# Kernel optimization log

Hardware: AMD Instinct MI355X
Metric: run time of the kernel (lower is better)

Reference implementation:

```python
import jax, jax.numpy as jnp
import numpy as np

# dims
B, N, DEG = 128, 512, 8          # graphs per batch, nodes per graph, avg degree
NL, F1, F2, F3 = 32, 128, 96, 64  # label dim, GCN filter sizes
K, BINS, BN = 16, 16, 32          # tensor_neurons, bins, bottle_neck_neurons
NT = B * N                        # total nodes per side
E = NT * DEG                      # total edges per side


def setup_inputs() -> dict:
    key = jax.random.key(0)
    ks = jax.random.split(key, 24)
    x1 = jax.random.normal(ks[0], (NT, NL), jnp.float32)
    x2 = jax.random.normal(ks[1], (NT, NL), jnp.float32)
    # edges constrained to stay within each graph's node block
    src1 = jax.random.randint(ks[2], (E,), 0, NT)
    dst1 = (src1 // N) * N + jax.random.randint(ks[3], (E,), 0, N)
    src2 = jax.random.randint(ks[4], (E,), 0, NT)
    dst2 = (src2 // N) * N + jax.random.randint(ks[5], (E,), 0, N)
    edge_index_1 = jnp.stack([src1, dst1]).astype(jnp.int32)
    edge_index_2 = jnp.stack([src2, dst2]).astype(jnp.int32)
    batch = jnp.repeat(jnp.arange(B, dtype=jnp.int32), N)
    s = 0.1
    params = dict(
        Wc1=jax.random.normal(ks[6], (NL, F1), jnp.float32) * s,
        bc1=jnp.zeros((F1,), jnp.float32),
        Wc2=jax.random.normal(ks[7], (F1, F2), jnp.float32) * s,
        bc2=jnp.zeros((F2,), jnp.float32),
        Wc3=jax.random.normal(ks[8], (F2, F3), jnp.float32) * s,
        bc3=jnp.zeros((F3,), jnp.float32),
        Watt=jax.random.normal(ks[9], (F3, F3), jnp.float32) * s,
        Wt=jax.random.normal(ks[10], (F3, F3, K), jnp.float32) * s,
        Wtb=jax.random.normal(ks[11], (K, 2 * F3), jnp.float32) * s,
        tb=jnp.zeros((K,), jnp.float32),
        W1=jax.random.normal(ks[12], (K + BINS, BN), jnp.float32) * s,
        b1=jnp.zeros((BN,), jnp.float32),
        Ws=jax.random.normal(ks[13], (BN, 1), jnp.float32) * s,
        bs=jnp.zeros((1,), jnp.float32),
    )
    return dict(x1=x1, x2=x2, edge_index_1=edge_index_1, edge_index_2=edge_index_2,
                batch_1=batch, batch_2=batch, **params)


def gcn_layer(x, src, dst, W, b):
    # PyG GCNConv: out = D^{-1/2}(A+I)D^{-1/2} (x W) + b
    n = x.shape[0]
    deg = jax.ops.segment_sum(jnp.ones(src.shape[0], x.dtype), dst, num_segments=n) + 1.0
    dinv = jax.lax.rsqrt(deg)
    h = x @ W
    norm = dinv[src] * dinv[dst]
    agg = jax.ops.segment_sum(h[src] * norm[:, None], dst, num_segments=n)
    agg = agg + h * (dinv * dinv)[:, None]  # self-loop term
    return agg + b


def conv_pass(x, src, dst, Wc1, bc1, Wc2, bc2, Wc3, bc3):
    h = jax.nn.relu(gcn_layer(x, src, dst, Wc1, bc1))  # dropout is identity in eval
    h = jax.nn.relu(gcn_layer(h, src, dst, Wc2, bc2))
    return gcn_layer(h, src, dst, Wc3, bc3)


def attention_pool(x, batch, Watt):
    # SimGNN attention: sigmoid(x . tanh(mean_g(x) W)) weighted sum per graph
    cnt = jax.ops.segment_sum(jnp.ones(x.shape[0], x.dtype), batch, num_segments=B)
    mean = jax.ops.segment_sum(x, batch, num_segments=B) / cnt[:, None]
    ctx = jnp.tanh(mean @ Watt)                       # [B, F3]
    coef = jax.nn.sigmoid(jnp.sum(x * ctx[batch], -1))  # [NT]
    return jax.ops.segment_sum(x * coef[:, None], batch, num_segments=B)


def histogram(f1, f2):
    # all graphs have exactly N nodes -> dense batch is a reshape, num_nodes=N
    f1d = f1.reshape(B, N, F3)
    f2d = f2.reshape(B, N, F3)
    s = jax.lax.stop_gradient(jnp.einsum('bnf,bmf->bnm', f1d, f2d))  # detach
    v = jax.nn.sigmoid(s).reshape(B, N * N)
    vmin = v.min(1, keepdims=True)
    vmax = v.max(1, keepdims=True)
    width = (vmax - vmin) / BINS  # torch.histc with min=max=0 uses data range
    safe = jnp.where(width > 0, width, 1.0)
    idx = jnp.clip(jnp.floor((v - vmin) / safe), 0, BINS - 1).astype(jnp.int32)
    flat = (idx + jnp.arange(B, dtype=jnp.int32)[:, None] * BINS).reshape(-1)
    hist = jax.ops.segment_sum(jnp.ones(B * N * N, v.dtype), flat,
                               num_segments=B * BINS).reshape(B, BINS)
    return hist / hist.sum(1, keepdims=True)


def reference(x1, x2, edge_index_1, edge_index_2, batch_1, batch_2,
              Wc1, bc1, Wc2, bc2, Wc3, bc3, Watt, Wt, Wtb, tb, W1, b1, Ws, bs):
    f1 = conv_pass(x1, edge_index_1[0], edge_index_1[1], Wc1, bc1, Wc2, bc2, Wc3, bc3)
    f2 = conv_pass(x2, edge_index_2[0], edge_index_2[1], Wc1, bc1, Wc2, bc2, Wc3, bc3)
    hist = histogram(f1, f2)
    p1 = attention_pool(f1, batch_1, Watt)
    p2 = attention_pool(f2, batch_2, Watt)
    # tensor network: e1^T W[:,:,k] e2 + Wtb [e1;e2] + b
    scoring = jnp.einsum('bi,ijk,bj->bk', p1, Wt, p2)
    block = jnp.concatenate([p1, p2], axis=1) @ Wtb.T
    t = jax.nn.relu(scoring + block + tb)             # [B, K]
    feat = jnp.concatenate([t, hist], axis=1)         # [B, K+BINS]
    h = jax.nn.relu(feat @ W1 + b1)
    return jax.nn.sigmoid(h @ Ws + bs).reshape(-1)    # [B]
```

## Files before the change

### kernel.cpp

```cpp
#include <hip/hip_runtime.h>
#include <math.h>

#define NTOT  65536
#define NEDGE 524288
#define BGR   128
#define NPG   512
#define NL    32
#define F1    128
#define F2    96
#define F3    64
#define KT    16
#define BINS  16
#define BN    32
#define GCAP  6144

typedef unsigned short bf;
typedef __attribute__((ext_vector_type(8))) short sv8;
typedef __attribute__((ext_vector_type(16))) float fv16;

__device__ __forceinline__ float b2f(bf v) { return __uint_as_float(((unsigned)v) << 16); }
__device__ __forceinline__ bf f2b(float f) {
    unsigned u = __float_as_uint(f);
    return (bf)((u + 0x7FFF + ((u >> 16) & 1)) >> 16);
}
__device__ __forceinline__ float sigm(float x) { return 1.f / (1.f + expf(-x)); }

__global__ __launch_bounds__(256) void init_k(const float* __restrict__ W1, const float* __restrict__ W2,
                                              const float* __restrict__ W3,
                                              bf* __restrict__ T1, bf* __restrict__ T2, bf* __restrict__ T3,
                                              int* __restrict__ gcount) {
    int i = blockIdx.x * 256 + threadIdx.x;
    if (i < 256) gcount[i] = 0;
    if (i < NL * F1) {
        int co = i >> 5, ci = i & 31;
        T1[i] = f2b(W1[ci * F1 + co]);
    } else if (i < NL * F1 + F1 * F2) {
        int i2 = i - NL * F1;
        int co = i2 >> 7, ci = i2 & 127;
        T2[i2] = f2b(W2[ci * F2 + co]);
    } else if (i < NL * F1 + F1 * F2 + F2 * F3) {
        int i3 = i - NL * F1 - F1 * F2;
        int co = i3 / 96, ci = i3 - co * 96;
        T3[i3] = f2b(W3[ci * F3 + co]);
    }
}

__global__ __launch_bounds__(256) void bucket_k(const int* __restrict__ ei1, const int* __restrict__ ei2,
                                                int* __restrict__ gcount, unsigned* __restrict__ bucket) {
    int side = blockIdx.y;
    const int* src = side ? ei2 : ei1;
    const int* dst = src + NEDGE;
    __shared__ int bc[128], bbase[128], bcur[128];
    int t = threadIdx.x;
    if (t < 128) { bc[t] = 0; bcur[t] = 0; }
    __syncthreads();
    int e0 = blockIdx.x * 1024;
    unsigned lp[4];
    int lg[4];
#pragma unroll
    for (int i = 0; i < 4; i++) {
        int e = e0 + i * 256 + t;
        int s = src[e], d = dst[e];
        int g = d >> 9;
        lp[i] = ((unsigned)s << 9) | (unsigned)(d & 511);
        lg[i] = g;
        atomicAdd(&bc[g], 1);
    }
    __syncthreads();
    if (t < 128 && bc[t] > 0) bbase[t] = atomicAdd(&gcount[side * 128 + t], bc[t]);
    __syncthreads();
#pragma unroll
    for (int i = 0; i < 4; i++) {
        int g = lg[i];
        int pos = bbase[g] + atomicAdd(&bcur[g], 1);
        if (pos < GCAP) bucket[((size_t)side * 128 + g) * GCAP + pos] = lp[i];
    }
}

__global__ void gscan_k(const int* __restrict__ gcount, int* __restrict__ gbase) {
    __shared__ int s[256];
    int t = threadIdx.x;
    int x = gcount[t];
    s[t] = x;
    __syncthreads();
    for (int o = 1; o < 128; o <<= 1) {
        int v = ((t & 127) >= o) ? s[t - o] : 0;
        __syncthreads();
        s[t] += v;
        __syncthreads();
    }
    gbase[t] = (t >> 7) * NEDGE + s[t] - x;
}

__global__ __launch_bounds__(256) void csr_k(const unsigned* __restrict__ bucket, const int* __restrict__ gcount,
                                             const int* __restrict__ gbase, int* __restrict__ off,
                                             float* __restrict__ dinv, unsigned* __restrict__ ecsr) {
    int side = blockIdx.y, g = blockIdx.x, t = threadIdx.x;
    __shared__ int ncnt[512];
    __shared__ int c2[256];
    __shared__ int cur[512];
    __shared__ float dloc[512];
    ncnt[t] = 0; ncnt[t + 256] = 0;
    __syncthreads();
    int cnt = gcount[side * 128 + g];
    cnt = cnt < GCAP ? cnt : GCAP;
    int base = gbase[side * 128 + g];
    const unsigned* bk = bucket + ((size_t)side * 128 + g) * GCAP;
    for (int i = t; i < cnt; i += 256) atomicAdd(&ncnt[bk[i] & 511], 1);
    __syncthreads();
    int e0 = ncnt[2 * t], e1 = ncnt[2 * t + 1];
    c2[t] = e0 + e1;
    __syncthreads();
    for (int o = 1; o < 256; o <<= 1) {
        int v = (t >= o) ? c2[t - o] : 0;
        __syncthreads();
        c2[t] += v;
        __syncthreads();
    }
    int ex = c2[t] - (e0 + e1);
    cur[2 * t] = ex;
    cur[2 * t + 1] = ex + e0;
    float d0 = rsqrtf((float)e0 + 1.f), d1 = rsqrtf((float)e1 + 1.f);
    dloc[2 * t] = d0; dloc[2 * t + 1] = d1;
    int node0 = g * NPG + 2 * t;
    int* offs = off + side * (NTOT + 1);
    offs[node0] = base + ex;
    offs[node0 + 1] = base + ex + e0;
    *(float2*)(dinv + (size_t)side * NTOT + node0) = make_float2(d0, d1);
    if (g == BGR - 1 && t == 0) offs[NTOT] = (side + 1) * NEDGE;
    __syncthreads();
    for (int i = t; i < cnt; i += 256) {
        unsigned p = bk[i];
        int dl = p & 511;
        int s = p >> 9;
        int pos = atomicAdd(&cur[dl], 1);
        float nm = dloc[s & 511] * dloc[dl];
        ecsr[base + pos] = (unsigned)s | ((unsigned)f2b(nm) << 16);
    }
}

__global__ __launch_bounds__(256) void aggemm1_k(const float* __restrict__ x1, const float* __restrict__ x2,
                                                 const int* __restrict__ off, const unsigned* __restrict__ ecsr,
                                                 const float* __restrict__ dinv,
                                                 const bf* __restrict__ wt1, const float* __restrict__ bias,
                                                 bf* __restrict__ outb) {
    int side = blockIdx.y;
    const float* x = side ? x2 : x1;
    const int* offs = off + side * (NTOT + 1);
    const float* dv = dinv + (size_t)side * NTOT;
    bf* out = outb + (size_t)side * NTOT * F1;
    int wave = threadIdx.x >> 6, lane = threadIdx.x & 63;
    int half = lane >> 5, r = lane & 31;
    int row0 = blockIdx.x * 128 + wave * 32;
    int n = row0 + r;
    int g0 = (n >> 9) << 9;
    float z[16];
    float d = dv[n];
    float sc = d * d;
    const float* xr = x + (size_t)n * NL + half * 8;
#pragma unroll
    for (int ks = 0; ks < 2; ks++) {
        float4 v0 = *(const float4*)(xr + ks * 16);
        float4 v1 = *(const float4*)(xr + ks * 16 + 4);
        z[ks * 8 + 0] = v0.x * sc; z[ks * 8 + 1] = v0.y * sc;
        z[ks * 8 + 2] = v0.z * sc; z[ks * 8 + 3] = v0.w * sc;
        z[ks * 8 + 4] = v1.x * sc; z[ks * 8 + 5] = v1.y * sc;
        z[ks * 8 + 6] = v1.z * sc; z[ks * 8 + 7] = v1.w * sc;
    }
    int e0 = offs[n], e1 = offs[n + 1];
    for (int j = e0; j < e1; j++) {
        unsigned en = ecsr[j];
        int s = en & 0xFFFF;
        float w = b2f((bf)(en >> 16));
        const float* xs = x + (size_t)s * NL + half * 8;
#pragma unroll
        for (int ks = 0; ks < 2; ks++) {
            float4 u0 = *(const float4*)(xs + ks * 16);
            float4 u1 = *(const float4*)(xs + ks * 16 + 4);
            z[ks * 8 + 0] += w * u0.x; z[ks * 8 + 1] += w * u0.y;
            z[ks * 8 + 2] += w * u0.z; z[ks * 8 + 3] += w * u0.w;
            z[ks * 8 + 4] += w * u1.x; z[ks * 8 + 5] += w * u1.y;
            z[ks * 8 + 6] += w * u1.z; z[ks * 8 + 7] += w * u1.w;
        }
    }
    (void)g0;
    sv8 a0, a1;
#pragma unroll
    for (int jj = 0; jj < 8; jj++) {
        a0[jj] = (short)f2b(z[jj]);
        a1[jj] = (short)f2b(z[8 + jj]);
    }
#pragma unroll
    for (int nt = 0; nt < F1 / 32; nt++) {
        const bf* Bp = wt1 + (size_t)(nt * 32 + r) * NL + half * 8;
        sv8 b0 = *(const sv8*)(Bp);
        sv8 b1 = *(const sv8*)(Bp + 16);
        fv16 acc;
#pragma unroll
        for (int i = 0; i < 16; i++) acc[i] = 0.f;
        acc = __builtin_amdgcn_mfma_f32_32x32x16_bf16(a0, b0, acc, 0, 0, 0);
        acc = __builtin_amdgcn_mfma_f32_32x32x16_bf16(a1, b1, acc, 0, 0, 0);
        float bv = bias[nt * 32 + r];
#pragma unroll
        for (int i = 0; i < 16; i++) {
            int rr = (i & 3) + 8 * (i >> 2) + 4 * half;
            float v = fmaxf(acc[i] + bv, 0.f);
            out[(size_t)(row0 + rr) * F1 + nt * 32 + r] = f2b(v);
        }
    }
}

template <int CIN, int COUT, int BIAS, int RELU>
__global__ __launch_bounds__(256) void gemmm_k(const bf* __restrict__ Xb, const bf* __restrict__ Wt,
                                               const float* __restrict__ bias, bf* __restrict__ outb) {
    int side = blockIdx.y;
    const bf* X = Xb + (size_t)side * NTOT * CIN;
    bf* out = outb + (size_t)side * NTOT * COUT;
    int wave = threadIdx.x >> 6, lane = threadIdx.x & 63;
    int half = lane >> 5, r = lane & 31;
    int row0 = blockIdx.x * 128 + wave * 32;
    const bf* Ap = X + (size_t)(row0 + r) * CIN + half * 8;
    sv8 a[CIN / 16];
#pragma unroll
    for (int k = 0; k < CIN / 16; k++) a[k] = *(const sv8*)(Ap + k * 16);
#pragma unroll
    for (int nt = 0; nt < COUT / 32; nt++) {
        const bf* Bp = Wt + (size_t)(nt * 32 + r) * CIN + half * 8;
        fv16 acc;
#pragma unroll
        for (int i = 0; i < 16; i++) acc[i] = 0.f;
#pragma unroll
        for (int k = 0; k < CIN / 16; k++)
            acc = __builtin_amdgcn_mfma_f32_32x32x16_bf16(a[k], *(const sv8*)(Bp + k * 16), acc, 0, 0, 0);
        float bv = BIAS ? bias[nt * 32 + r] : 0.f;
#pragma unroll
        for (int i = 0; i < 16; i++) {
            int rr = (i & 3) + 8 * (i >> 2) + 4 * half;
            float v = acc[i] + bv;
            if (RELU) v = fmaxf(v, 0.f);
            out[(size_t)(row0 + rr) * COUT + nt * 32 + r] = f2b(v);
        }
    }
}

template <int C, int RELU>
__global__ __launch_bounds__(256) void agg_k(const bf* __restrict__ hinb, const float* __restrict__ bias,
                                             const int* __restrict__ off, const unsigned* __restrict__ ecsr,
                                             const float* __restrict__ dinv, bf* __restrict__ outb) {
    constexpr int C4 = C / 4;
    int side = blockIdx.y;
    const bf* hin = hinb + (size_t)side * NTOT * C;
    bf* out = outb + (size_t)side * NTOT * C;
    const int* offs = off + side * (NTOT + 1);
    int t = blockIdx.x * 256 + threadIdx.x;
    int node = t / C4;
    int c = (t % C4) * 4;
    float d = dinv[(size_t)side * NTOT + node];
    float sc = d * d;
    ushort4 h = *(const ushort4*)(hin + (size_t)node * C + c);
    float ax = b2f(h.x) * sc, ay = b2f(h.y) * sc, az = b2f(h.z) * sc, aw = b2f(h.w) * sc;
    int e0 = offs[node], e1 = offs[node + 1];
    int j = e0;
    for (; j + 2 <= e1; j += 2) {
        unsigned ena = ecsr[j], enb = ecsr[j + 1];
        int sa = ena & 0xFFFF, sb = enb & 0xFFFF;
        float wa = b2f((bf)(ena >> 16)), wb = b2f((bf)(enb >> 16));
        ushort4 ha = *(const ushort4*)(hin + (size_t)sa * C + c);
        ushort4 hb = *(const ushort4*)(hin + (size_t)sb * C + c);
        ax += wa * b2f(ha.x) + wb * b2f(hb.x);
        ay += wa * b2f(ha.y) + wb * b2f(hb.y);
        az += wa * b2f(ha.z) + wb * b2f(hb.z);
        aw += wa * b2f(ha.w) + wb * b2f(hb.w);
    }
    if (j < e1) {
        unsigned en = ecsr[j];
        int s = en & 0xFFFF;
        float w = b2f((bf)(en >> 16));
        ushort4 hs = *(const ushort4*)(hin + (size_t)s * C + c);
        ax += w * b2f(hs.x); ay += w * b2f(hs.y); az += w * b2f(hs.z); aw += w * b2f(hs.w);
    }
    float4 bv = *(const float4*)(bias + c);
    ax += bv.x; ay += bv.y; az += bv.z; aw += bv.w;
    if (RELU) {
        ax = fmaxf(ax, 0.f); ay = fmaxf(ay, 0.f); az = fmaxf(az, 0.f); aw = fmaxf(aw, 0.f);
    }
    ushort4 o;
    o.x = f2b(ax); o.y = f2b(ay); o.z = f2b(az); o.w = f2b(aw);
    *(ushort4*)(out + (size_t)node * C + c) = o;
}

template <int C>
__global__ __launch_bounds__(256) void aggf_k(const bf* __restrict__ hinb, const float* __restrict__ bias,
                                              const int* __restrict__ off, const unsigned* __restrict__ ecsr,
                                              const float* __restrict__ dinv,
                                              bf* __restrict__ f1, bf* __restrict__ f2) {
    constexpr int C4 = C / 4;
    int side = blockIdx.y;
    const bf* hin = hinb + (size_t)side * NTOT * C;
    bf* out = side ? f2 : f1;
    const int* offs = off + side * (NTOT + 1);
    int t = blockIdx.x * 256 + threadIdx.x;
    int node = t / C4;
    int c = (t % C4) * 4;
    float d = dinv[(size_t)side * NTOT + node];
    float sc = d * d;
    ushort4 h = *(const ushort4*)(hin + (size_t)node * C + c);
    float ax = b2f(h.x) * sc, ay = b2f(h.y) * sc, az = b2f(h.z) * sc, aw = b2f(h.w) * sc;
    int e0 = offs[node], e1 = offs[node + 1];
    int j = e0;
    for (; j + 2 <= e1; j += 2) {
        unsigned ena = ecsr[j], enb = ecsr[j + 1];
        int sa = ena & 0xFFFF, sb = enb & 0xFFFF;
        float wa = b2f((bf)(ena >> 16)), wb = b2f((bf)(enb >> 16));
        ushort4 ha = *(const ushort4*)(hin + (size_t)sa * C + c);
        ushort4 hb = *(const ushort4*)(hin + (size_t)sb * C + c);
        ax += wa * b2f(ha.x) + wb * b2f(hb.x);
        ay += wa * b2f(ha.y) + wb * b2f(hb.y);
        az += wa * b2f(ha.z) + wb * b2f(hb.z);
        aw += wa * b2f(ha.w) + wb * b2f(hb.w);
    }
    if (j < e1) {
        unsigned en = ecsr[j];
        int s = en & 0xFFFF;
        float w = b2f((bf)(en >> 16));
        ushort4 hs = *(const ushort4*)(hin + (size_t)s * C + c);
        ax += w * b2f(hs.x); ay += w * b2f(hs.y); az += w * b2f(hs.z); aw += w * b2f(hs.w);
    }
    float4 bv = *(const float4*)(bias + c);
    ax += bv.x; ay += bv.y; az += bv.z; aw += bv.w;
    ushort4 o;
    o.x = f2b(ax); o.y = f2b(ay); o.z = f2b(az); o.w = f2b(aw);
    *(ushort4*)(out + (size_t)node * C + c) = o;
}

__device__ __forceinline__ void sim_tile(const bf* __restrict__ f1, const bf* __restrict__ f2,
                                         int g, int mt, int wave, int lane, fv16 acc[4]) {
    int half = lane >> 5, r = lane & 31;
    const bf* Ap = f1 + ((size_t)g * NPG + mt * 32 + r) * F3 + half * 8;
    sv8 a0 = *(const sv8*)(Ap +  0);
    sv8 a1 = *(const sv8*)(Ap + 16);
    sv8 a2 = *(const sv8*)(Ap + 32);
    sv8 a3 = *(const sv8*)(Ap + 48);
#pragma unroll
    for (int j = 0; j < 4; j++) {
        int nt = j * 4 + wave;
        const bf* Bp = f2 + ((size_t)g * NPG + nt * 32 + r) * F3 + half * 8;
#pragma unroll
        for (int i = 0; i < 16; i++) acc[j][i] = 0.f;
        acc[j] = __builtin_amdgcn_mfma_f32_32x32x16_bf16(a0, *(const sv8*)(Bp +  0), acc[j], 0, 0, 0);
        acc[j] = __builtin_amdgcn_mfma_f32_32x32x16_bf16(a1, *(const sv8*)(Bp + 16), acc[j], 0, 0, 0);
        acc[j] = __builtin_amdgcn_mfma_f32_32x32x16_bf16(a2, *(const sv8*)(Bp + 32), acc[j], 0, 0, 0);
        acc[j] = __builtin_amdgcn_mfma_f32_32x32x16_bf16(a3, *(const sv8*)(Bp + 48), acc[j], 0, 0, 0);
    }
}

__global__ __launch_bounds__(256) void simmean_k(const bf* __restrict__ f1, const bf* __restrict__ f2,
                                                 float* __restrict__ statmin, float* __restrict__ statmax,
                                                 float* __restrict__ meanp) {
    __shared__ float red[256];
    int bid = blockIdx.x;
    int t = threadIdx.x, wave = t >> 6, lane = t & 63;
    if (bid < 2048) {
        int g = bid >> 4, mt = bid & 15;
        fv16 acc[4];
        sim_tile(f1, f2, g, mt, wave, lane, acc);
        float mn = 1e30f, mx = -1e30f;
#pragma unroll
        for (int j = 0; j < 4; j++)
#pragma unroll
            for (int i = 0; i < 16; i++) {
                mn = fminf(mn, acc[j][i]);
                mx = fmaxf(mx, acc[j][i]);
            }
        for (int o = 32; o; o >>= 1) {
            mn = fminf(mn, __shfl_down(mn, o));
            mx = fmaxf(mx, __shfl_down(mx, o));
        }
        if (lane == 0) { red[wave] = mn; red[4 + wave] = mx; }
        __syncthreads();
        if (t == 0) {
            statmin[g * 16 + mt] = fminf(fminf(red[0], red[1]), fminf(red[2], red[3]));
            statmax[g * 16 + mt] = fmaxf(fmaxf(red[4], red[5]), fmaxf(red[6], red[7]));
        }
    } else {
        int idx = bid - 2048;
        int side = idx >> 10, rem = idx & 1023;
        int ch = rem >> 7, g = rem & 127;
        const bf* xp = (side ? f2 : f1) + ((size_t)g * NPG + ch * 64) * F3;
        int f = t & 63;
        float m = 0.f;
#pragma unroll 4
        for (int i = 0; i < 16; i++) m += b2f(xp[(size_t)(wave * 16 + i) * F3 + f]);
        red[t] = m;
        __syncthreads();
        if (t < 64) meanp[(((size_t)side * BGR + g) * 8 + ch) * 64 + t] =
            red[t] + red[64 + t] + red[128 + t] + red[192 + t];
    }
}

__global__ __launch_bounds__(256) void simhctx_k(const bf* __restrict__ f1, const bf* __restrict__ f2,
                                                 const float* __restrict__ statmin, const float* __restrict__ statmax,
                                                 int* __restrict__ hist_p,
                                                 const float* __restrict__ meanp, const float* __restrict__ Watt,
                                                 float* __restrict__ ctxb) {
    __shared__ int ph[256 * 17];
    __shared__ int pr[256];
    int bid = blockIdx.x;
    int t = threadIdx.x, wave = t >> 6, lane = t & 63;
    if (bid < 2048) {
        int g = bid >> 4, mt = bid & 15;
#pragma unroll
        for (int b = 0; b < BINS; b++) ph[t * 17 + b] = 0;
        float pm = (lane < 16) ? statmin[g * 16 + lane] : 1e30f;
        float px = (lane < 16) ? statmax[g * 16 + lane] : -1e30f;
        for (int o = 8; o; o >>= 1) {
            pm = fminf(pm, __shfl_down(pm, o));
            px = fmaxf(px, __shfl_down(px, o));
        }
        float vmin = sigm(__shfl(pm, 0));
        float vmax = sigm(__shfl(px, 0));
        float width = (vmax - vmin) / (float)BINS;
        float inv = 1.0f / (width > 0.f ? width : 1.0f);
        fv16 acc[4];
        sim_tile(f1, f2, g, mt, wave, lane, acc);
#pragma unroll
        for (int j = 0; j < 4; j++)
#pragma unroll
            for (int i = 0; i < 16; i++) {
                float v = sigm(acc[j][i]);
                int bi = (int)floorf((v - vmin) * inv);
                bi = bi < 0 ? 0 : (bi > BINS - 1 ? BINS - 1 : bi);
                ph[t * 17 + bi] += 1;
            }
        __syncthreads();
        {
            int grp = t >> 4, bin = t & 15;
            int s = 0;
#pragma unroll
            for (int j = 0; j < 16; j++) s += ph[(grp * 16 + j) * 17 + bin];
            pr[t] = s;
        }
        __syncthreads();
        if (t < BINS) {
            int tot = 0;
#pragma unroll
            for (int j = 0; j < 16; j++) tot += pr[j * 16 + t];
            hist_p[((size_t)g * 16 + mt) * BINS + t] = tot;
        }
    } else {
        int idx = bid - 2048;
        int side = idx >> 7, g = idx & 127;
        float* sm = (float*)pr;
        if (t < 64) {
            float m = 0.f;
#pragma unroll
            for (int ch = 0; ch < 8; ch++) m += meanp[(((size_t)side * BGR + g) * 8 + ch) * 64 + t];
            sm[t] = m * (1.0f / (float)NPG);
        }
        __syncthreads();
        if (t < 64) {
            float acc = 0.f;
#pragma unroll 8
            for (int i = 0; i < F3; i++) acc += sm[i] * Watt[i * F3 + t];
            ctxb[((size_t)side * BGR + g) * F3 + t] = tanhf(acc);
        }
    }
}

__global__ __launch_bounds__(256) void cpool_k(const bf* __restrict__ f1, const bf* __restrict__ f2,
                                               const float* __restrict__ ctxb, float* __restrict__ poolp) {
    int g = blockIdx.x, ch = blockIdx.y, side = blockIdx.z;
    const bf* xp = (side ? f2 : f1) + ((size_t)g * NPG + ch * 64) * F3;
    int t = threadIdx.x, w = t >> 6, f = t & 63;
    float cx = ctxb[((size_t)side * BGR + g) * F3 + f];
    float acc = 0.f;
    for (int i = 0; i < 16; i++) {
        float v = b2f(xp[(size_t)(w * 16 + i) * F3 + f]);
        float d = v * cx;
#pragma unroll
        for (int o = 1; o < 64; o <<= 1) d += __shfl_xor(d, o);
        acc += sigm(d) * v;
    }
    __shared__ float red[256];
    red[t] = acc;
    __syncthreads();
    if (t < 64) poolp[(((size_t)side * BGR + g) * 8 + ch) * 64 + t] =
        red[t] + red[64 + t] + red[128 + t] + red[192 + t];
}

__global__ __launch_bounds__(256) void final_k(const float* __restrict__ poolp,
                                               const float* __restrict__ Wt, const float* __restrict__ Wtb,
                                               const float* __restrict__ tb, const int* __restrict__ hist_p,
                                               const float* __restrict__ W1, const float* __restrict__ b1,
                                               const float* __restrict__ Ws, const float* __restrict__ bs,
                                               float* __restrict__ out) {
    int b = blockIdx.x, t = threadIdx.x;
    __shared__ float cat[128];
    __shared__ float sacc[256];
    __shared__ float feat[32];
    __shared__ float hb[32];
    if (t < 128) {
        int side = t >> 6, f = t & 63;
        float s = 0.f;
#pragma unroll
        for (int ch = 0; ch < 8; ch++) s += poolp[(((size_t)side * BGR + b) * 8 + ch) * 64 + f];
        cat[t] = s;
    }
    __syncthreads();
    int k = t & 15, c = t >> 4;
    float acc = 0.f;
    for (int q = 0; q < 256; q++) {
        int ij = c * 256 + q;
        int i = ij >> 6, j = ij & 63;
        acc += cat[i] * cat[64 + j] * Wt[ij * KT + k];
    }
    sacc[t] = acc;
    __syncthreads();
    if (t < KT) {
        float sc = 0.f;
        for (int c2 = 0; c2 < 16; c2++) sc += sacc[c2 * 16 + t];
        float bt = 0.f;
        for (int i = 0; i < 128; i++) bt += cat[i] * Wtb[t * 128 + i];
        float tv = sc + bt + tb[t];
        feat[t] = tv > 0.f ? tv : 0.f;
        int hsum = 0;
#pragma unroll
        for (int j = 0; j < 16; j++) hsum += hist_p[((size_t)b * 16 + j) * BINS + t];
        feat[KT + t] = (float)hsum * (1.0f / (float)(NPG * NPG));
    }
    __syncthreads();
    if (t < BN) {
        float a = 0.f;
        for (int i = 0; i < KT + BINS; i++) a += feat[i] * W1[i * BN + t];
        a += b1[t];
        hb[t] = a > 0.f ? a : 0.f;
    }
    __syncthreads();
    if (t == 0) {
        float s = bs[0];
        for (int j = 0; j < BN; j++) s += hb[j] * Ws[j];
        out[b] = sigm(s);
    }
}

extern "C" void kernel_launch(void* const* d_in, const int* in_sizes, int n_in,
                              void* d_out, int out_size, void* d_ws, size_t ws_size,
                              hipStream_t stream) {
    const float* x1   = (const float*)d_in[0];
    const float* x2   = (const float*)d_in[1];
    const int*   ei1  = (const int*)d_in[2];
    const int*   ei2  = (const int*)d_in[3];
    const float* Wc1  = (const float*)d_in[6];
    const float* bc1  = (const float*)d_in[7];
    const float* Wc2  = (const float*)d_in[8];
    const float* bc2  = (const float*)d_in[9];
    const float* Wc3  = (const float*)d_in[10];
    const float* bc3  = (const float*)d_in[11];
    const float* Watt = (const float*)d_in[12];
    const float* Wt   = (const float*)d_in[13];
    const float* Wtb  = (const float*)d_in[14];
    const float* tb   = (const float*)d_in[15];
    const float* W1   = (const float*)d_in[16];
    const float* b1   = (const float*)d_in[17];
    const float* Ws   = (const float*)d_in[18];
    const float* bs   = (const float*)d_in[19];
    float* out = (float*)d_out;

    char* wsb = (char*)d_ws;
    size_t o = 0;
    auto alloc = [&](size_t bytes) -> void* {
        void* p = wsb + o;
        o = (o + bytes + 255) & ~(size_t)255;
        return p;
    };
    bf* f1b  = (bf*)alloc((size_t)NTOT * F3 * 2);
    bf* f2b  = (bf*)alloc((size_t)NTOT * F3 * 2);
    bf* X    = (bf*)alloc((size_t)2 * NTOT * F1 * 2);
    bf* Y    = (bf*)alloc((size_t)2 * NTOT * F2 * 2);
    int* off   = (int*)alloc((size_t)2 * (NTOT + 1) * 4);
    unsigned* ecsr = (unsigned*)alloc((size_t)2 * NEDGE * 4);
    unsigned* bucket = (unsigned*)alloc((size_t)2 * 128 * GCAP * 4);
    int* gcount = (int*)alloc(256 * 4);
    int* gbase  = (int*)alloc(256 * 4);
    float* dinv = (float*)alloc((size_t)2 * NTOT * 4);
    float* statmin = (float*)alloc((size_t)BGR * 16 * 4);
    float* statmax = (float*)alloc((size_t)BGR * 16 * 4);
    int* hist_p = (int*)alloc((size_t)BGR * 16 * BINS * 4);
    float* meanp = (float*)alloc((size_t)2 * BGR * 8 * 64 * 4);
    float* ctx   = (float*)alloc((size_t)2 * BGR * F3 * 4);
    float* poolp = (float*)alloc((size_t)2 * BGR * 8 * 64 * 4);
    bf* wt1 = (bf*)alloc((size_t)NL * F1 * 2);
    bf* wt2 = (bf*)alloc((size_t)F1 * F2 * 2);
    bf* wt3 = (bf*)alloc((size_t)F2 * F3 * 2);
    (void)ws_size; (void)in_sizes; (void)n_in; (void)out_size;

    init_k<<<(NL * F1 + F1 * F2 + F2 * F3 + 255) / 256, 256, 0, stream>>>(Wc1, Wc2, Wc3, wt1, wt2, wt3, gcount);

    bucket_k<<<dim3(NEDGE / 1024, 2), 256, 0, stream>>>(ei1, ei2, gcount, bucket);
    gscan_k<<<1, 256, 0, stream>>>(gcount, gbase);
    csr_k<<<dim3(BGR, 2), 256, 0, stream>>>(bucket, gcount, gbase, off, dinv, ecsr);

    aggemm1_k<<<dim3(NTOT / 128, 2), 256, 0, stream>>>(x1, x2, off, ecsr, dinv, wt1, bc1, X);
    gemmm_k<F1, F2, 0, 0><<<dim3(NTOT / 128, 2), 256, 0, stream>>>(X, wt2, nullptr, Y);
    agg_k<F2, 1><<<dim3((NTOT * (F2 / 4)) / 256, 2), 256, 0, stream>>>(Y, bc2, off, ecsr, dinv, X);
    gemmm_k<F2, F3, 0, 0><<<dim3(NTOT / 128, 2), 256, 0, stream>>>(X, wt3, nullptr, Y);
    aggf_k<F3><<<dim3((NTOT * (F3 / 4)) / 256, 2), 256, 0, stream>>>(Y, bc3, off, ecsr, dinv, f1b, f2b);

    simmean_k<<<4096, 256, 0, stream>>>(f1b, f2b, statmin, statmax, meanp);
    simhctx_k<<<2048 + 256, 256, 0, stream>>>(f1b, f2b, statmin, statmax, hist_p, meanp, Watt, ctx);
    cpool_k<<<dim3(BGR, 8, 2), 256, 0, stream>>>(f1b, f2b, ctx, poolp);

    final_k<<<BGR, 256, 0, stream>>>(poolp, Wt, Wtb, tb, hist_p, W1, b1, Ws, bs, out);
}
```

Baseline: 350.6 us.

## Fuse layer-1 aggregate+GEMM with layer-2 GEMM and fold group scan into CSR

Layer 1's aggregation and GEMM now feed their ReLU output through a shared-memory tile straight into the layer-2 weight GEMM. The 128-wide bf16 intermediate no longer round-trips through global memory, and one kernel launch is dropped. The separate single-block group prefix scan is removed; each CSR block recomputes the 128-entry scan in shared memory. The cost is 34KB of LDS per block, which may lower occupancy, plus some redundant scan work per block.

```diff
diff --git a/kernel.cpp b/kernel.cpp
--- a/kernel.cpp
+++ b/kernel.cpp
@@ -77,34 +77,27 @@
     }
 }
 
-__global__ void gscan_k(const int* __restrict__ gcount, int* __restrict__ gbase) {
-    __shared__ int s[256];
-    int t = threadIdx.x;
-    int x = gcount[t];
-    s[t] = x;
-    __syncthreads();
-    for (int o = 1; o < 128; o <<= 1) {
-        int v = ((t & 127) >= o) ? s[t - o] : 0;
-        __syncthreads();
-        s[t] += v;
-        __syncthreads();
-    }
-    gbase[t] = (t >> 7) * NEDGE + s[t] - x;
-}
-
 __global__ __launch_bounds__(256) void csr_k(const unsigned* __restrict__ bucket, const int* __restrict__ gcount,
-                                             const int* __restrict__ gbase, int* __restrict__ off,
-                                             float* __restrict__ dinv, unsigned* __restrict__ ecsr) {
+                                             int* __restrict__ off, float* __restrict__ dinv,
+                                             unsigned* __restrict__ ecsr) {
     int side = blockIdx.y, g = blockIdx.x, t = threadIdx.x;
     __shared__ int ncnt[512];
     __shared__ int c2[256];
     __shared__ int cur[512];
     __shared__ float dloc[512];
+    __shared__ int gs[128];
     ncnt[t] = 0; ncnt[t + 256] = 0;
-    __syncthreads();
+    if (t < 128) gs[t] = gcount[side * 128 + t];
+    __syncthreads();
+    for (int o = 1; o < 128; o <<= 1) {
+        int v = (t >= o && t < 128) ? gs[t - o] : 0;
+        __syncthreads();
+        if (t < 128) gs[t] += v;
+        __syncthreads();
+    }
     int cnt = gcount[side * 128 + g];
     cnt = cnt < GCAP ? cnt : GCAP;
-    int base = gbase[side * 128 + g];
+    int base = side * NEDGE + (g > 0 ? gs[g - 1] : 0);
     const unsigned* bk = bucket + ((size_t)side * 128 + g) * GCAP;
     for (int i = t; i < cnt; i += 256) atomicAdd(&ncnt[bk[i] & 511], 1);
     __syncthreads();
@@ -139,21 +132,22 @@
     }
 }
 
-__global__ __launch_bounds__(256) void aggemm1_k(const float* __restrict__ x1, const float* __restrict__ x2,
-                                                 const int* __restrict__ off, const unsigned* __restrict__ ecsr,
-                                                 const float* __restrict__ dinv,
-                                                 const bf* __restrict__ wt1, const float* __restrict__ bias,
-                                                 bf* __restrict__ outb) {
+#define HSTR 136
+__global__ __launch_bounds__(256) void aggemm12_k(const float* __restrict__ x1, const float* __restrict__ x2,
+                                                  const int* __restrict__ off, const unsigned* __restrict__ ecsr,
+                                                  const float* __restrict__ dinv,
+                                                  const bf* __restrict__ wt1, const float* __restrict__ bc1,
+                                                  const bf* __restrict__ wt2, bf* __restrict__ Yb) {
+    __shared__ bf Hs[128 * HSTR];
     int side = blockIdx.y;
     const float* x = side ? x2 : x1;
     const int* offs = off + side * (NTOT + 1);
     const float* dv = dinv + (size_t)side * NTOT;
-    bf* out = outb + (size_t)side * NTOT * F1;
+    bf* Y = Yb + (size_t)side * NTOT * F2;
     int wave = threadIdx.x >> 6, lane = threadIdx.x & 63;
     int half = lane >> 5, r = lane & 31;
     int row0 = blockIdx.x * 128 + wave * 32;
     int n = row0 + r;
-    int g0 = (n >> 9) << 9;
     float z[16];
     float d = dv[n];
     float sc = d * d;
@@ -183,7 +177,6 @@
             z[ks * 8 + 6] += w * u1.z; z[ks * 8 + 7] += w * u1.w;
         }
     }
-    (void)g0;
     sv8 a0, a1;
 #pragma unroll
     for (int jj = 0; jj < 8; jj++) {
@@ -200,12 +193,30 @@
         for (int i = 0; i < 16; i++) acc[i] = 0.f;
         acc = __builtin_amdgcn_mfma_f32_32x32x16_bf16(a0, b0, acc, 0, 0, 0);
         acc = __builtin_amdgcn_mfma_f32_32x32x16_bf16(a1, b1, acc, 0, 0, 0);
-        float bv = bias[nt * 32 + r];
+        float bv = bc1[nt * 32 + r];
 #pragma unroll
         for (int i = 0; i < 16; i++) {
             int rr = (i & 3) + 8 * (i >> 2) + 4 * half;
-            float v = fmaxf(acc[i] + bv, 0.f);
-            out[(size_t)(row0 + rr) * F1 + nt * 32 + r] = f2b(v);
+            Hs[(wave * 32 + rr) * HSTR + nt * 32 + r] = f2b(fmaxf(acc[i] + bv, 0.f));
+        }
+    }
+    sv8 a[8];
+#pragma unroll
+    for (int k = 0; k < 8; k++)
+        a[k] = *(const sv8*)&Hs[(wave * 32 + r) * HSTR + k * 16 + half * 8];
+#pragma unroll
+    for (int nt = 0; nt < F2 / 32; nt++) {
+        const bf* Bp = wt2 + (size_t)(nt * 32 + r) * F1 + half * 8;
+        fv16 acc;
+#pragma unroll
+        for (int i = 0; i < 16; i++) acc[i] = 0.f;
+#pragma unroll
+        for (int k = 0; k < 8; k++)
+            acc = __builtin_amdgcn_mfma_f32_32x32x16_bf16(a[k], *(const sv8*)(Bp + k * 16), acc, 0, 0, 0);
+#pragma unroll
+        for (int i = 0; i < 16; i++) {
+            int rr = (i & 3) + 8 * (i >> 2) + 4 * half;
+            Y[(size_t)(row0 + rr) * F2 + nt * 32 + r] = f2b(acc[i]);
         }
     }
 }
@@ -575,13 +586,12 @@
     };
     bf* f1b  = (bf*)alloc((size_t)NTOT * F3 * 2);
     bf* f2b  = (bf*)alloc((size_t)NTOT * F3 * 2);
-    bf* X    = (bf*)alloc((size_t)2 * NTOT * F1 * 2);
+    bf* X    = (bf*)alloc((size_t)2 * NTOT * F2 * 2);
     bf* Y    = (bf*)alloc((size_t)2 * NTOT * F2 * 2);
     int* off   = (int*)alloc((size_t)2 * (NTOT + 1) * 4);
     unsigned* ecsr = (unsigned*)alloc((size_t)2 * NEDGE * 4);
     unsigned* bucket = (unsigned*)alloc((size_t)2 * 128 * GCAP * 4);
     int* gcount = (int*)alloc(256 * 4);
-    int* gbase  = (int*)alloc(256 * 4);
     float* dinv = (float*)alloc((size_t)2 * NTOT * 4);
     float* statmin = (float*)alloc((size_t)BGR * 16 * 4);
     float* statmax = (float*)alloc((size_t)BGR * 16 * 4);
@@ -597,11 +607,9 @@
     init_k<<<(NL * F1 + F1 * F2 + F2 * F3 + 255) / 256, 256, 0, stream>>>(Wc1, Wc2, Wc3, wt1, wt2, wt3, gcount);
 
     bucket_k<<<dim3(NEDGE / 1024, 2), 256, 0, stream>>>(ei1, ei2, gcount, bucket);
-    gscan_k<<<1, 256, 0, stream>>>(gcount, gbase);
-    csr_k<<<dim3(BGR, 2), 256, 0, stream>>>(bucket, gcount, gbase, off, dinv, ecsr);
-
-    aggemm1_k<<<dim3(NTOT / 128, 2), 256, 0, stream>>>(x1, x2, off, ecsr, dinv, wt1, bc1, X);
-    gemmm_k<F1, F2, 0, 0><<<dim3(NTOT / 128, 2), 256, 0, stream>>>(X, wt2, nullptr, Y);
+    csr_k<<<dim3(BGR, 2), 256, 0, stream>>>(bucket, gcount, off, dinv, ecsr);
+
+    aggemm12_k<<<dim3(NTOT / 128, 2), 256, 0, stream>>>(x1, x2, off, ecsr, dinv, wt1, bc1, wt2, Y);
     agg_k<F2, 1><<<dim3((NTOT * (F2 / 4)) / 256, 2), 256, 0, stream>>>(Y, bc2, off, ecsr, dinv, X);
     gemmm_k<F2, F3, 0, 0><<<dim3(NTOT / 128, 2), 256, 0, stream>>>(X, wt3, nullptr, Y);
     aggf_k<F3><<<dim3((NTOT * (F3 / 4)) / 256, 2), 256, 0, stream>>>(Y, bc3, off, ecsr, dinv, f1b, f2b);
```

Result: faster. 339.7 us (-3.1%).
